# Kernel optimization log

Measured on AMD Instinct MI355X. Metric: run time of the kernel, lower is better.

The kernel has to match this reference:

```python
import jax, jax.numpy as jnp
import numpy as np

B, LATENT, HID, OUT, E = 8192, 128, 400, 4096, 16

def setup_inputs() -> dict:
    key = jax.random.key(0)
    k = jax.random.split(key, 6)
    return {
        "z": jax.random.normal(k[0], (B, LATENT), dtype=jnp.float32),
        "W1": jax.random.normal(k[1], (E, HID, LATENT), dtype=jnp.float32) * (1.0 / np.sqrt(LATENT)),
        "b1": jax.random.normal(k[2], (E, HID), dtype=jnp.float32) * 0.01,
        "W2": jax.random.normal(k[3], (E, OUT, HID), dtype=jnp.float32) * (1.0 / np.sqrt(HID)),
        "b2": jax.random.normal(k[4], (E, OUT), dtype=jnp.float32) * 0.01,
        "angle_idx": jax.random.randint(k[5], (B,), 0, E, dtype=jnp.int64) if jax.config.jax_enable_x64 else jax.random.randint(k[5], (B,), 0, E, dtype=jnp.int32),
    }

def reference(z, W1, b1, W2, b2, angle_idx):
    # Per-sample expert select: out[i] = sigmoid(W2[e] @ relu(W1[e] @ z[i] + b1[e]) + b2[e]), e = angle_idx[i].
    # Dense-dispatch reference: run every expert on the full batch, select per-sample result.
    n_experts = W1.shape[0]
    out = jnp.zeros((z.shape[0], W2.shape[1]), dtype=z.dtype)
    for e in range(n_experts):  # small fixed loop over experts
        h = jax.nn.relu(z @ W1[e].T + b1[e])          # [B, 400]
        o = jax.nn.sigmoid(h @ W2[e].T + b2[e])       # [B, OUT]
        out = jnp.where((angle_idx == e)[:, None], o, out)
    return out
```

## Files before the change

### kernel.cpp

```cpp
#include <hip/hip_runtime.h>

#define BATCH  8192
#define LATENT 128
#define HID    400
#define HIDB   400
#define HIDP   448
#define NOUT   4096
#define NE     16
#define HROWS  (BATCH + 256)

typedef __attribute__((ext_vector_type(8))) short bf16x8;
typedef __attribute__((ext_vector_type(4))) float f32x4;

__device__ __forceinline__ unsigned short f2bf(float f){
  unsigned u = __builtin_bit_cast(unsigned, f);
  u += 0x7fffu + ((u >> 16) & 1u);
  return (unsigned short)(u >> 16);
}

__device__ __forceinline__ void gload16(const void* g, void* l){
  __builtin_amdgcn_global_load_lds(
      (const __attribute__((address_space(1))) void*)g,
      (__attribute__((address_space(3))) void*)l, 16, 0, 0);
}

__global__ __launch_bounds__(1024) void k_prep(
    const int* __restrict__ aidx, int* __restrict__ wsI,
    const float* __restrict__ W2, unsigned short* __restrict__ W2b)
{
  int tid = threadIdx.x;
  if (blockIdx.x != 0){
    const int NCH = NE*NOUT*HIDB/8;
    int g = ((int)blockIdx.x - 1)*1024 + tid;
    for (int i = g; i < NCH; i += 1536*1024){
      const float* s = W2 + (size_t)i*8;
      f32x4 a = __builtin_nontemporal_load((const f32x4*)s);
      f32x4 b = __builtin_nontemporal_load((const f32x4*)(s+4));
      bf16x8 w;
      w[0]=(short)f2bf(a.x); w[1]=(short)f2bf(a.y); w[2]=(short)f2bf(a.z); w[3]=(short)f2bf(a.w);
      w[4]=(short)f2bf(b.x); w[5]=(short)f2bf(b.y); w[6]=(short)f2bf(b.z); w[7]=(short)f2bf(b.w);
      __builtin_nontemporal_store(w, (bf16x8*)(W2b + (size_t)i*8));
    }
    return;
  }
  __shared__ int hist[NE];
  __shared__ int cursor[NE];
  int lane = tid & 63;
  if (tid < NE) hist[tid] = 0;
  __syncthreads();

  int ev[8];
  #pragma unroll
  for (int c=0;c<8;c++) ev[c] = aidx[c*1024 + tid];

  #pragma unroll
  for (int c=0;c<8;c++){
    for (int x=0;x<NE;x++){
      unsigned long long m = __ballot(ev[c]==x);
      if (lane==0 && m) atomicAdd(&hist[x], (int)__popcll(m));
    }
  }
  __syncthreads();
  if (tid==0){
    int a=0;
    for (int x=0;x<NE;x++){ cursor[x]=a; wsI[32+x]=a; a+=hist[x]; }
    wsI[32+NE]=a;
  }
  __syncthreads();

  #pragma unroll
  for (int c=0;c<8;c++){
    int e = ev[c], i = c*1024 + tid;
    for (int x=0;x<NE;x++){
      unsigned long long m = __ballot(e==x);
      if (m){
        int leader = __ffsll((unsigned long long)m) - 1;
        int base = 0;
        if (lane == leader) base = atomicAdd(&cursor[x], (int)__popcll(m));
        base = __shfl(base, leader);
        if (e==x){
          int rank = (int)__popcll(m & ((1ull<<lane)-1ull));
          wsI[64 + base + rank] = i;
        }
      }
    }
  }
}

__global__ __launch_bounds__(256) void k_layer1(
    const float* __restrict__ z, const float* __restrict__ W1, const float* __restrict__ b1,
    const int* __restrict__ wsI, unsigned short* __restrict__ hws)
{
  __shared__ int s_off[NE+1];
  __shared__ int s_perm[64];
  __shared__ unsigned short As[64*128];
  __shared__ unsigned short Bs[64*128];
  int tid = threadIdx.x;
  if (tid <= NE) s_off[tid] = wsI[32+tid];
  __syncthreads();

  int e=-1, tile=0;
  { int acc=0;
    for (int i=0;i<NE;i++){
      int cnt = s_off[i+1]-s_off[i]; int t = (cnt+63)>>6;
      if ((int)blockIdx.x < acc+t){ e=i; tile=(int)blockIdx.x-acc; break; }
      acc += t; } }
  if (e < 0) return;
  int r0 = s_off[e] + tile*64;
  int rows = s_off[e+1] - r0; if (rows > 64) rows = 64;
  int n0 = blockIdx.y * 64;

  if (tid < 64) s_perm[tid] = (tid < rows) ? wsI[64 + r0 + tid] : 0;
  __syncthreads();

  #pragma unroll
  for (int p=0;p<8;p++){
    int id = tid + p*256; int row = id>>5, c4 = id&31;
    float4 v = make_float4(0.f,0.f,0.f,0.f);
    if (row < rows) v = *(const float4*)(z + (size_t)s_perm[row]*LATENT + c4*4);
    short4 w; w.x=(short)f2bf(v.x); w.y=(short)f2bf(v.y); w.z=(short)f2bf(v.z); w.w=(short)f2bf(v.w);
    *(short4*)((char*)As + row*256 + ((c4*8) ^ ((row&7)<<4))) = w;
  }
  const float* w1e = W1 + (size_t)e*HID*LATENT;
  #pragma unroll
  for (int p=0;p<8;p++){
    int id = tid + p*256; int row = id>>5, c4 = id&31;
    int n = n0 + row;
    float4 v = make_float4(0.f,0.f,0.f,0.f);
    if (n < HID) v = *(const float4*)(w1e + (size_t)n*LATENT + c4*4);
    short4 w; w.x=(short)f2bf(v.x); w.y=(short)f2bf(v.y); w.z=(short)f2bf(v.z); w.w=(short)f2bf(v.w);
    *(short4*)((char*)Bs + row*256 + ((c4*8) ^ ((row&7)<<4))) = w;
  }
  __syncthreads();

  int lane = tid & 63, wid = tid >> 6;
  int wm = wid >> 1, wn = wid & 1;
  int llo = lane & 15, lhi = lane >> 4;
  f32x4 acc[2][2];
  #pragma unroll
  for (int i=0;i<2;i++)
    #pragma unroll
    for (int j=0;j<2;j++) acc[i][j] = (f32x4){0.f,0.f,0.f,0.f};

  #pragma unroll
  for (int s=0;s<4;s++){
    bf16x8 af[2], bfr[2];
    #pragma unroll
    for (int i=0;i<2;i++){ int m = wm*32 + i*16 + llo;
      af[i] = *(bf16x8*)((char*)As + m*256 + ((s*64 + lhi*16) ^ ((m&7)<<4))); }
    #pragma unroll
    for (int j=0;j<2;j++){ int n = wn*32 + j*16 + llo;
      bfr[j] = *(bf16x8*)((char*)Bs + n*256 + ((s*64 + lhi*16) ^ ((n&7)<<4))); }
    #pragma unroll
    for (int i=0;i<2;i++)
      #pragma unroll
      for (int j=0;j<2;j++)
        acc[i][j] = __builtin_amdgcn_mfma_f32_16x16x32_bf16(af[i], bfr[j], acc[i][j], 0,0,0);
  }

  const float* b1e = b1 + e*HID;
  #pragma unroll
  for (int i=0;i<2;i++){
    #pragma unroll
    for (int j=0;j<2;j++){
      int n = n0 + wn*32 + j*16 + llo;
      float bias = (n < HID) ? b1e[n] : 0.f;
      #pragma unroll
      for (int q=0;q<4;q++){
        int m = wm*32 + i*16 + lhi*4 + q;
        if (m < rows){
          float v = acc[i][j][q] + bias;
          v = (v > 0.f) ? v : 0.f;
          if (n >= HID) v = 0.f;
          hws[(size_t)(r0+m)*HIDP + n] = f2bf(v);
        }
      }
    }
  }
}

__global__ __launch_bounds__(256) void k_layer2(
    const unsigned short* __restrict__ hws, const unsigned short* __restrict__ W2b,
    const float* __restrict__ b2, const int* __restrict__ wsI, float* __restrict__ out)
{
  __shared__ int s_off[NE+1];
  __shared__ int s_perm[128];
  __shared__ unsigned short As[4][128*32];
  __shared__ unsigned short Bs[4][128*32];
  int tid = threadIdx.x;
  if (tid <= NE) s_off[tid] = wsI[32+tid];
  __syncthreads();

  int lin = (int)blockIdx.x;
  int logical = (lin & 7) * 320 + (lin >> 3);
  int bx = logical % 80, by = logical / 80;

  int e=-1, tile=0;
  { int acc=0;
    for (int i=0;i<NE;i++){
      int cnt = s_off[i+1]-s_off[i]; int t = (cnt+127)>>7;
      if (bx < acc+t){ e=i; tile=bx-acc; break; }
      acc += t; } }
  if (e < 0) return;
  int r0 = s_off[e] + tile*128;
  int rows = s_off[e+1] - r0; if (rows > 128) rows = 128;
  int n0 = by * 128;
  if (tid < 128) s_perm[tid] = (tid < rows) ? wsI[64 + r0 + tid] : 0;

  const unsigned short* aBase[2];
  const unsigned short* bBase[2];
  #pragma unroll
  for (int p=0;p<2;p++){
    int a = tid + p*256; int r = a>>2, u = a&3;
    int cu = u ^ ((r>>1)&3);
    aBase[p] = hws + (size_t)(r0 + r)*HIDP + cu*8;
    bBase[p] = W2b + ((size_t)e*NOUT + n0 + r)*HIDB + cu*8;
  }

  int lane = tid & 63, w = tid >> 6;
  int wm = w >> 1, wn = w & 1;
  int llo = lane & 15, lhi = lane >> 4;
  f32x4 acc[4][4];
  #pragma unroll
  for (int i=0;i<4;i++)
    #pragma unroll
    for (int j=0;j<4;j++) acc[i][j] = (f32x4){0.f,0.f,0.f,0.f};

  #define STAGE(T) { \
    _Pragma("unroll") for (int p=0;p<2;p++){ \
      int a = tid + p*256; \
      gload16(aBase[p] + (T)*32, &As[(T)&3][a*8]); \
      gload16(bBase[p] + (T)*32, &Bs[(T)&3][a*8]); } }

  STAGE(0); STAGE(1);

  for (int kt=0; kt<13; kt++){
    if (kt < 11){
      STAGE(kt+2);
      asm volatile("s_waitcnt vmcnt(8)" ::: "memory");
    } else if (kt == 11){
      asm volatile("s_waitcnt vmcnt(4)" ::: "memory");
    } else {
      asm volatile("s_waitcnt vmcnt(0)" ::: "memory");
    }
    __builtin_amdgcn_s_barrier();

    const char* Ab = (const char*)&As[kt&3][0];
    const char* Bb = (const char*)&Bs[kt&3][0];
    bf16x8 af[4], bfr[4];
    #pragma unroll
    for (int i=0;i<4;i++){ int m = wm*64 + i*16 + llo;
      af[i] = *(bf16x8*)(Ab + m*64 + ((lhi*16) ^ (((m>>1)&3)<<4))); }
    #pragma unroll
    for (int j=0;j<4;j++){ int n = wn*64 + j*16 + llo;
      bfr[j] = *(bf16x8*)(Bb + n*64 + ((lhi*16) ^ (((n>>1)&3)<<4)));
      if (kt == 12 && lhi >= 2) bfr[j] = (bf16x8){0,0,0,0,0,0,0,0};
    }
    #pragma unroll
    for (int i=0;i<4;i++)
      #pragma unroll
      for (int j=0;j<4;j++)
        acc[i][j] = __builtin_amdgcn_mfma_f32_16x16x32_bf16(af[i], bfr[j], acc[i][j], 0,0,0);
  }

  const float* b2e = b2 + (size_t)e*NOUT;
  #pragma unroll
  for (int i=0;i<4;i++){
    int mb = wm*64 + i*16 + lhi*4;
    #pragma unroll
    for (int q=0;q<4;q++){
      int m = mb + q;
      if (m < rows){
        int orow = s_perm[m];
        float* op = out + (size_t)orow*NOUT + n0;
        #pragma unroll
        for (int j=0;j<4;j++){
          int nloc = wn*64 + j*16 + llo;
          float x = acc[i][j][q] + b2e[n0 + nloc];
          __builtin_nontemporal_store(1.f / (1.f + __expf(-x)), op + nloc);
        }
      }
    }
  }
}

extern "C" void kernel_launch(void* const* d_in, const int* in_sizes, int n_in,
                              void* d_out, int out_size, void* d_ws, size_t ws_size,
                              hipStream_t stream){
  const float* z   = (const float*)d_in[0];
  const float* W1  = (const float*)d_in[1];
  const float* b1  = (const float*)d_in[2];
  const float* W2  = (const float*)d_in[3];
  const float* b2  = (const float*)d_in[4];
  const int*  aidx = (const int*)d_in[5];
  float* out = (float*)d_out;
  int* wsI = (int*)d_ws;
  unsigned short* hws = (unsigned short*)((char*)d_ws + 65536);
  unsigned short* W2b = (unsigned short*)((char*)d_ws + 65536 + (size_t)HROWS*HIDP*2);

  k_prep  <<<1537, 1024, 0, stream>>>(aidx, wsI, W2, W2b);
  k_layer1<<<dim3(144, 7), 256, 0, stream>>>(z, W1, b1, wsI, hws);
  k_layer2<<<2560, 256, 0, stream>>>(hws, W2b, b2, wsI, out);
}
```

Before: 165.6 us.

## Load layer-2 activations directly into registers and double-buffer weights with wider K tiles

The layer-2 GEMM no longer stages the hidden activations through LDS. Each wave loads its A fragments straight from global memory into registers with inline asm. The weight tile is now double-buffered in LDS with 64-wide K steps (7 iterations instead of 13), and the last step overlaps K to cover the 400-wide hidden dimension. This removes LDS traffic and barriers for A and halves the loop trip count, in exchange for redundant global reads of A across waves and hand-tuned waitcnt accounting. The last tile reads up to column 448, which relies on the zero-padded activation columns 400-447.

```diff
diff --git a/kernel.cpp b/kernel.cpp
--- a/kernel.cpp
+++ b/kernel.cpp
@@ -11,6 +11,7 @@
 
 typedef __attribute__((ext_vector_type(8))) short bf16x8;
 typedef __attribute__((ext_vector_type(4))) float f32x4;
+typedef __attribute__((ext_vector_type(2))) unsigned u32x2;
 
 __device__ __forceinline__ unsigned short f2bf(float f){
   unsigned u = __builtin_bit_cast(unsigned, f);
@@ -185,8 +186,7 @@
 {
   __shared__ int s_off[NE+1];
   __shared__ int s_perm[128];
-  __shared__ unsigned short As[4][128*32];
-  __shared__ unsigned short Bs[4][128*32];
+  __shared__ unsigned short Bs[2][128*64];
   int tid = threadIdx.x;
   if (tid <= NE) s_off[tid] = wsI[32+tid];
   __syncthreads();
@@ -207,60 +207,85 @@
   int n0 = by * 128;
   if (tid < 128) s_perm[tid] = (tid < rows) ? wsI[64 + r0 + tid] : 0;
 
-  const unsigned short* aBase[2];
-  const unsigned short* bBase[2];
-  #pragma unroll
-  for (int p=0;p<2;p++){
-    int a = tid + p*256; int r = a>>2, u = a&3;
-    int cu = u ^ ((r>>1)&3);
-    aBase[p] = hws + (size_t)(r0 + r)*HIDP + cu*8;
-    bBase[p] = W2b + ((size_t)e*NOUT + n0 + r)*HIDB + cu*8;
-  }
-
   int lane = tid & 63, w = tid >> 6;
   int wm = w >> 1, wn = w & 1;
   int llo = lane & 15, lhi = lane >> 4;
+
+  int srow = lane >> 3;
+  int colU = (lane & 7) ^ srow;
+  const unsigned short* bSrcBase = W2b + ((size_t)e*NOUT + n0)*HIDB + colU*8;
+  int bAdj = (colU >= 2) ? (336 - 384) : 0;
+
+  u32x2 pA[4];
+  #pragma unroll
+  for (int i=0;i<4;i++){
+    int m = wm*64 + i*16 + llo;
+    const unsigned short* p = hws + (size_t)(r0 + m)*HIDP + lhi*8;
+    unsigned long long a = (unsigned long long)p;
+    pA[i] = (u32x2){(unsigned)a, (unsigned)(a>>32)};
+  }
+
   f32x4 acc[4][4];
   #pragma unroll
   for (int i=0;i<4;i++)
     #pragma unroll
     for (int j=0;j<4;j++) acc[i][j] = (f32x4){0.f,0.f,0.f,0.f};
 
-  #define STAGE(T) { \
-    _Pragma("unroll") for (int p=0;p<2;p++){ \
-      int a = tid + p*256; \
-      gload16(aBase[p] + (T)*32, &As[(T)&3][a*8]); \
-      gload16(bBase[p] + (T)*32, &Bs[(T)&3][a*8]); } }
-
-  STAGE(0); STAGE(1);
-
-  for (int kt=0; kt<13; kt++){
-    if (kt < 11){
-      STAGE(kt+2);
+  #define STAGE_B(BUF, K0, ADJ) { _Pragma("unroll") for (int p=0;p<4;p++){ \
+      int c = w*4 + p; int row = c*8 + srow; \
+      gload16(bSrcBase + (size_t)row*HIDB + (K0) + (ADJ), &Bs[BUF][c*512]); } }
+
+  STAGE_B(0, 0, 0);
+
+  int cur = 0;
+  for (int kt=0; kt<7; kt++){
+    f32x4 a0[4], a1[4];
+    #pragma unroll
+    for (int i=0;i<4;i++){
+      asm volatile("global_load_dwordx4 %0, %2, off\n\t"
+                   "global_load_dwordx4 %1, %2, off offset:64"
+                   : "=&v"(a0[i]), "=&v"(a1[i]) : "v"(pA[i]) : "memory");
+    }
+    if (kt < 6){
+      if (kt == 5){ STAGE_B(cur^1, 384, bAdj); }
+      else        { STAGE_B(cur^1, (kt+1)*64, 0); }
+      asm volatile("s_waitcnt vmcnt(12)" ::: "memory");
+    } else {
       asm volatile("s_waitcnt vmcnt(8)" ::: "memory");
-    } else if (kt == 11){
-      asm volatile("s_waitcnt vmcnt(4)" ::: "memory");
-    } else {
-      asm volatile("s_waitcnt vmcnt(0)" ::: "memory");
-    }
+    }
+    __builtin_amdgcn_sched_barrier(0);
     __builtin_amdgcn_s_barrier();
 
-    const char* Ab = (const char*)&As[kt&3][0];
-    const char* Bb = (const char*)&Bs[kt&3][0];
-    bf16x8 af[4], bfr[4];
-    #pragma unroll
-    for (int i=0;i<4;i++){ int m = wm*64 + i*16 + llo;
-      af[i] = *(bf16x8*)(Ab + m*64 + ((lhi*16) ^ (((m>>1)&3)<<4))); }
-    #pragma unroll
-    for (int j=0;j<4;j++){ int n = wn*64 + j*16 + llo;
-      bfr[j] = *(bf16x8*)(Bb + n*64 + ((lhi*16) ^ (((n>>1)&3)<<4)));
-      if (kt == 12 && lhi >= 2) bfr[j] = (bf16x8){0,0,0,0,0,0,0,0};
-    }
-    #pragma unroll
-    for (int i=0;i<4;i++)
+    bf16x8 bfr[2][4];
+    #pragma unroll
+    for (int s=0;s<2;s++)
       #pragma unroll
-      for (int j=0;j<4;j++)
-        acc[i][j] = __builtin_amdgcn_mfma_f32_16x16x32_bf16(af[i], bfr[j], acc[i][j], 0,0,0);
+      for (int j=0;j<4;j++){ int n = wn*64 + j*16 + llo;
+        bfr[s][j] = *(bf16x8*)((char*)&Bs[cur][0] + n*128 + ((s*64 + lhi*16) ^ ((n&7)<<4))); }
+
+    if (kt < 6) asm volatile("s_waitcnt vmcnt(4)" ::: "memory");
+    else        asm volatile("s_waitcnt vmcnt(0)" ::: "memory");
+    __builtin_amdgcn_sched_barrier(0);
+
+    #pragma unroll
+    for (int i=0;i<4;i++){
+      bf16x8 afc0 = __builtin_bit_cast(bf16x8, a0[i]);
+      bf16x8 afc1 = __builtin_bit_cast(bf16x8, a1[i]);
+      #pragma unroll
+      for (int j=0;j<4;j++){
+        acc[i][j] = __builtin_amdgcn_mfma_f32_16x16x32_bf16(afc0, bfr[0][j], acc[i][j], 0,0,0);
+        acc[i][j] = __builtin_amdgcn_mfma_f32_16x16x32_bf16(afc1, bfr[1][j], acc[i][j], 0,0,0);
+      }
+    }
+    __builtin_amdgcn_s_barrier();
+
+    #pragma unroll
+    for (int i=0;i<4;i++){
+      unsigned long long a = ((unsigned long long)pA[i].y << 32) | pA[i].x;
+      a += 128;
+      pA[i] = (u32x2){(unsigned)a, (unsigned)(a>>32)};
+    }
+    cur ^= 1;
   }
 
   const float* b2e = b2 + (size_t)e*NOUT;
```

New measurement: 188.0 us. +13.5%, slower.

## Use 64-wide K tiles with double buffering in layer-2 GEMM

Applied to the files above, without the earlier changes.

Restructures the layer-2 K loop from 13 steps of 32-wide K with a 4-deep LDS ring into 7 steps of 64-wide K with two LDS buffers. Each step now runs two MFMA sub-steps. Global-to-LDS loads use a new 8-row XOR swizzle. The last tile reuses shifted in-range W2 columns against zeroed hidden columns instead of masking fragments in registers. The aim is fewer barriers and waits per unit of work, at the cost of a shallower prefetch pipeline and an extra barrier per iteration.

```diff
diff --git a/kernel.cpp b/kernel.cpp
--- a/kernel.cpp
+++ b/kernel.cpp
@@ -185,8 +185,8 @@
 {
   __shared__ int s_off[NE+1];
   __shared__ int s_perm[128];
-  __shared__ unsigned short As[4][128*32];
-  __shared__ unsigned short Bs[4][128*32];
+  __shared__ unsigned short As[2][128*64];
+  __shared__ unsigned short Bs[2][128*64];
   int tid = threadIdx.x;
   if (tid <= NE) s_off[tid] = wsI[32+tid];
   __syncthreads();
@@ -207,17 +207,13 @@
   int n0 = by * 128;
   if (tid < 128) s_perm[tid] = (tid < rows) ? wsI[64 + r0 + tid] : 0;
 
-  const unsigned short* aBase[2];
-  const unsigned short* bBase[2];
-  #pragma unroll
-  for (int p=0;p<2;p++){
-    int a = tid + p*256; int r = a>>2, u = a&3;
-    int cu = u ^ ((r>>1)&3);
-    aBase[p] = hws + (size_t)(r0 + r)*HIDP + cu*8;
-    bBase[p] = W2b + ((size_t)e*NOUT + n0 + r)*HIDB + cu*8;
-  }
-
   int lane = tid & 63, w = tid >> 6;
+  int srow = lane >> 3;
+  int colU = (lane & 7) ^ srow;
+  const unsigned short* aSrcBase = hws + (size_t)r0*HIDP + colU*8;
+  const unsigned short* bSrcBase = W2b + ((size_t)e*NOUT + n0)*HIDB + colU*8;
+  int bAdj = (colU >= 2) ? -48 : 0;
+
   int wm = w >> 1, wn = w & 1;
   int llo = lane & 15, lhi = lane >> 4;
   f32x4 acc[4][4];
@@ -226,41 +222,39 @@
     #pragma unroll
     for (int j=0;j<4;j++) acc[i][j] = (f32x4){0.f,0.f,0.f,0.f};
 
-  #define STAGE(T) { \
-    _Pragma("unroll") for (int p=0;p<2;p++){ \
-      int a = tid + p*256; \
-      gload16(aBase[p] + (T)*32, &As[(T)&3][a*8]); \
-      gload16(bBase[p] + (T)*32, &Bs[(T)&3][a*8]); } }
-
-  STAGE(0); STAGE(1);
-
-  for (int kt=0; kt<13; kt++){
-    if (kt < 11){
-      STAGE(kt+2);
+  #define STAGE(BUF, K0, ADJ) { _Pragma("unroll") for (int p=0;p<4;p++){ \
+      int c = w*4 + p; int row = c*8 + srow; \
+      gload16(aSrcBase + (size_t)row*HIDP + (K0), &As[BUF][c*512]); \
+      gload16(bSrcBase + (size_t)row*HIDB + (K0) + (ADJ), &Bs[BUF][c*512]); } }
+
+  STAGE(0, 0, 0);
+
+  int cur = 0;
+  for (int kt=0; kt<7; kt++){
+    if (kt < 6){
+      STAGE(cur^1, (kt+1)*64, ((kt+1)==6) ? bAdj : 0);
       asm volatile("s_waitcnt vmcnt(8)" ::: "memory");
-    } else if (kt == 11){
-      asm volatile("s_waitcnt vmcnt(4)" ::: "memory");
     } else {
       asm volatile("s_waitcnt vmcnt(0)" ::: "memory");
     }
     __builtin_amdgcn_s_barrier();
-
-    const char* Ab = (const char*)&As[kt&3][0];
-    const char* Bb = (const char*)&Bs[kt&3][0];
-    bf16x8 af[4], bfr[4];
-    #pragma unroll
-    for (int i=0;i<4;i++){ int m = wm*64 + i*16 + llo;
-      af[i] = *(bf16x8*)(Ab + m*64 + ((lhi*16) ^ (((m>>1)&3)<<4))); }
-    #pragma unroll
-    for (int j=0;j<4;j++){ int n = wn*64 + j*16 + llo;
-      bfr[j] = *(bf16x8*)(Bb + n*64 + ((lhi*16) ^ (((n>>1)&3)<<4)));
-      if (kt == 12 && lhi >= 2) bfr[j] = (bf16x8){0,0,0,0,0,0,0,0};
-    }
-    #pragma unroll
-    for (int i=0;i<4;i++)
-      #pragma unroll
-      for (int j=0;j<4;j++)
-        acc[i][j] = __builtin_amdgcn_mfma_f32_16x16x32_bf16(af[i], bfr[j], acc[i][j], 0,0,0);
+    #pragma unroll
+    for (int s=0;s<2;s++){
+      bf16x8 af[4], bfr[4];
+      #pragma unroll
+      for (int i=0;i<4;i++){ int m = wm*64 + i*16 + llo;
+        af[i] = *(bf16x8*)((char*)&As[cur][0] + m*128 + ((s*64 + lhi*16) ^ ((m&7)<<4))); }
+      #pragma unroll
+      for (int j=0;j<4;j++){ int n = wn*64 + j*16 + llo;
+        bfr[j] = *(bf16x8*)((char*)&Bs[cur][0] + n*128 + ((s*64 + lhi*16) ^ ((n&7)<<4))); }
+      #pragma unroll
+      for (int i=0;i<4;i++)
+        #pragma unroll
+        for (int j=0;j<4;j++)
+          acc[i][j] = __builtin_amdgcn_mfma_f32_16x16x32_bf16(af[i], bfr[j], acc[i][j], 0,0,0);
+    }
+    __builtin_amdgcn_s_barrier();
+    cur ^= 1;
   }
 
   const float* b2e = b2 + (size_t)e*NOUT;
```

Result: faster. 161.6 us (-2.4%).
